# Optimization experiments

Measured on AMD Instinct MI355X. Metric: run time of the kernel, lower is better.

## Reference

```python
import jax, jax.numpy as jnp
import numpy as np

B, L1, L2, H, A = 32, 512, 512, 256, 256

def setup_inputs() -> dict:
    key = jax.random.key(0)
    ks = jax.random.split(key, 10)
    s = 0.05
    return {
        'x1': jax.random.normal(ks[0], (B, L1, H), jnp.float32),
        'x2': jax.random.normal(ks[1], (B, L2, H), jnp.float32),
        'w1': jax.random.normal(ks[2], (A, H), jnp.float32) * s,
        'w2': jax.random.normal(ks[3], (A, H), jnp.float32) * s,
        'D': jax.random.normal(ks[4], (A, A), jnp.float32) * s,
        'W': jax.random.normal(ks[5], (L1, L2), jnp.float32) * s,
        'gru_wih': jax.random.normal(ks[6], (3 * H, 2 * H), jnp.float32) * s,
        'gru_whh': jax.random.normal(ks[7], (3 * H, H), jnp.float32) * s,
        'gru_bih': jax.random.normal(ks[8], (3 * H,), jnp.float32) * s,
        'gru_bhh': jax.random.normal(ks[9], (3 * H,), jnp.float32) * s,
    }

def _gru(seq, wih, whh, bih, bhh):
    # seq: [B, T, 2H]; PyTorch GRU gate order: r, z, n
    h_dim = whh.shape[1]
    x_proj = seq @ wih.T + bih  # [B, T, 3H]
    x_proj = jnp.swapaxes(x_proj, 0, 1)  # [T, B, 3H]
    h0 = jnp.zeros((seq.shape[0], h_dim), seq.dtype)

    def step(h, xp):
        hp = h @ whh.T + bhh  # [B, 3H]
        xr, xz, xn = jnp.split(xp, 3, axis=-1)
        hr, hz, hn = jnp.split(hp, 3, axis=-1)
        r = jax.nn.sigmoid(xr + hr)
        z = jax.nn.sigmoid(xz + hz)
        n = jnp.tanh(xn + r * hn)
        h_new = (1.0 - z) * n + z * h
        return h_new, h_new

    _, out = jax.lax.scan(step, h0, x_proj)
    return jnp.swapaxes(out, 0, 1)  # [B, T, H]

def reference(x1, x2, w1, w2, D, W, gru_wih, gru_whh, gru_bih, gru_bhh):
    a1 = jax.nn.relu(x1 @ w1.T)            # [B, L1, A]
    a2 = jax.nn.relu(x2 @ w2.T)            # [B, L2, A]
    a1 = a1 @ D                             # [B, L1, A]
    M = jnp.einsum('bia,bja->bij', a1, a2)  # [B, L1, L2]
    M = M * W[None, :, :]
    M = jax.nn.softmax(M, axis=1)           # softmax over len1 axis (dim=1)
    ctx = jnp.einsum('bij,bjh->bih', M, x2) # [B, L1, H]
    g = jnp.concatenate([x1, ctx], axis=2)  # [B, L1, 2H]
    return _gru(g, gru_wih, gru_whh, gru_bih, gru_bhh)
```

## Files before the change

kernel.cpp:

```cpp
#include <hip/hip_runtime.h>
#include <hip/hip_bf16.h>
#include <cstdint>
#include <cstddef>


typedef short s8v __attribute__((ext_vector_type(8)));
typedef float f4v __attribute__((ext_vector_type(4)));
typedef _Float16 h8v __attribute__((ext_vector_type(8)));

#if __has_builtin(__builtin_amdgcn_sched_barrier)
#define SCHED_FENCE() __builtin_amdgcn_sched_barrier(0)
#else
#define SCHED_FENCE() asm volatile("" ::: "memory")
#endif

__device__ __forceinline__ void bar_lds() {
    asm volatile("s_waitcnt lgkmcnt(0)\n\ts_barrier" ::: "memory");
}

__device__ __forceinline__ float fast_exp(float x) {
#if __has_builtin(__builtin_amdgcn_exp2f)
    return __builtin_amdgcn_exp2f(x * 1.44269504f);
#else
    return __expf(x);
#endif
}
__device__ __forceinline__ float fast_rcp(float x) {
#if __has_builtin(__builtin_amdgcn_rcpf)
    return __builtin_amdgcn_rcpf(x);
#else
    return 1.f / x;
#endif
}
__device__ __forceinline__ float fast_sig(float x) { return fast_rcp(1.f + fast_exp(-x)); }
__device__ __forceinline__ float fast_tanh(float x) {
    return 1.f - 2.f * fast_rcp(1.f + fast_exp(2.f * x));
}

__global__ __launch_bounds__(256) void gemm_bf16(
    const __hip_bfloat16* __restrict__ A, int lda, long long sA,
    const __hip_bfloat16* __restrict__ B, int ldb, long long sB,
    void* __restrict__ C, int ldc, long long sC,
    int K,
    const float* __restrict__ bias,
    const float* __restrict__ emul, int ldmul,
    int relu, int accum, int out_bf16)
{
    __shared__ short As[128][40];
    __shared__ short Bs[128][40];

    const int tid  = threadIdx.x;
    const int wave = tid >> 6, lane = tid & 63;
    const int quad = lane >> 4, l16 = lane & 15;
    const int wrow = (wave >> 1) * 64, wcol = (wave & 1) * 64;
    const int m0 = blockIdx.y * 128, n0 = blockIdx.x * 128;

    const short* Ab = (const short*)A + (size_t)blockIdx.z * sA;
    const short* Bb = (const short*)B + (size_t)blockIdx.z * sB;

    f4v acc[4][4];
#pragma unroll
    for (int i = 0; i < 4; ++i)
#pragma unroll
        for (int j = 0; j < 4; ++j) acc[i][j] = 0.f;

    const int r0 = tid >> 2,        s0 = (tid & 3) * 8;
    const int r1 = (tid + 256) >> 2, s1 = ((tid + 256) & 3) * 8;

    for (int k0 = 0; k0 < K; k0 += 32) {
        *(s8v*)&As[r0][s0] = *(const s8v*)(Ab + (size_t)(m0 + r0) * lda + k0 + s0);
        *(s8v*)&As[r1][s1] = *(const s8v*)(Ab + (size_t)(m0 + r1) * lda + k0 + s1);
        *(s8v*)&Bs[r0][s0] = *(const s8v*)(Bb + (size_t)(n0 + r0) * ldb + k0 + s0);
        *(s8v*)&Bs[r1][s1] = *(const s8v*)(Bb + (size_t)(n0 + r1) * ldb + k0 + s1);
        __syncthreads();

        s8v af[4], bf[4];
#pragma unroll
        for (int i = 0; i < 4; ++i)
            af[i] = *(const s8v*)&As[wrow + i * 16 + l16][quad * 8];
#pragma unroll
        for (int j = 0; j < 4; ++j)
            bf[j] = *(const s8v*)&Bs[wcol + j * 16 + l16][quad * 8];
#pragma unroll
        for (int i = 0; i < 4; ++i)
#pragma unroll
            for (int j = 0; j < 4; ++j)
                acc[i][j] = __builtin_amdgcn_mfma_f32_16x16x32_bf16(
                    af[i], bf[j], acc[i][j], 0, 0, 0);
        __syncthreads();
    }

    float* Cf = (float*)C + (size_t)blockIdx.z * sC;
    __hip_bfloat16* Cb = (__hip_bfloat16*)C + (size_t)blockIdx.z * sC;
#pragma unroll
    for (int i = 0; i < 4; ++i)
#pragma unroll
        for (int j = 0; j < 4; ++j)
#pragma unroll
            for (int r = 0; r < 4; ++r) {
                const int m = m0 + wrow + i * 16 + quad * 4 + r;
                const int n = n0 + wcol + j * 16 + l16;
                float v = acc[i][j][r];
                if (bias)  v += bias[n];
                if (accum) v += Cf[(size_t)m * ldc + n];
                if (emul)  v *= emul[(size_t)m * ldmul + n];
                if (relu)  v = fmaxf(v, 0.f);
                if (out_bf16) Cb[(size_t)m * ldc + n] = __float2bfloat16(v);
                else          Cf[(size_t)m * ldc + n] = v;
            }
}

__global__ __launch_bounds__(256) void gemm_M(
    const __hip_bfloat16* __restrict__ A,
    const __hip_bfloat16* __restrict__ B,
    __hip_bfloat16* __restrict__ E,
    const float* __restrict__ Wm,
    float* __restrict__ S)
{
    __shared__ short As[128][40];
    __shared__ short Bs[128][40];

    const int tid  = threadIdx.x;
    const int wave = tid >> 6, lane = tid & 63;
    const int quad = lane >> 4, l16 = lane & 15;
    const int wrow = (wave >> 1) * 64, wcol = (wave & 1) * 64;
    const int m0 = blockIdx.y * 128, n0 = blockIdx.x * 128;

    const short* Ab = (const short*)A + (size_t)blockIdx.z * 131072;
    const short* Bb = (const short*)B + (size_t)blockIdx.z * 131072;

    f4v acc[4][4];
#pragma unroll
    for (int i = 0; i < 4; ++i)
#pragma unroll
        for (int j = 0; j < 4; ++j) acc[i][j] = 0.f;

    const int r0 = tid >> 2,        s0 = (tid & 3) * 8;
    const int r1 = (tid + 256) >> 2, s1 = ((tid + 256) & 3) * 8;

    for (int k0 = 0; k0 < 256; k0 += 32) {
        *(s8v*)&As[r0][s0] = *(const s8v*)(Ab + (size_t)(m0 + r0) * 256 + k0 + s0);
        *(s8v*)&As[r1][s1] = *(const s8v*)(Ab + (size_t)(m0 + r1) * 256 + k0 + s1);
        *(s8v*)&Bs[r0][s0] = *(const s8v*)(Bb + (size_t)(n0 + r0) * 256 + k0 + s0);
        *(s8v*)&Bs[r1][s1] = *(const s8v*)(Bb + (size_t)(n0 + r1) * 256 + k0 + s1);
        __syncthreads();

        s8v af[4], bf[4];
#pragma unroll
        for (int i = 0; i < 4; ++i)
            af[i] = *(const s8v*)&As[wrow + i * 16 + l16][quad * 8];
#pragma unroll
        for (int j = 0; j < 4; ++j)
            bf[j] = *(const s8v*)&Bs[wcol + j * 16 + l16][quad * 8];
#pragma unroll
        for (int i = 0; i < 4; ++i)
#pragma unroll
            for (int j = 0; j < 4; ++j)
                acc[i][j] = __builtin_amdgcn_mfma_f32_16x16x32_bf16(
                    af[i], bf[j], acc[i][j], 0, 0, 0);
        __syncthreads();
    }

    __hip_bfloat16* Eb = E + (size_t)blockIdx.z * 262144;
    float* Sb = S + blockIdx.z * 512;
#pragma unroll
    for (int j = 0; j < 4; ++j) {
        const int n = n0 + wcol + j * 16 + l16;
        float colsum = 0.f;
#pragma unroll
        for (int i = 0; i < 4; ++i)
#pragma unroll
            for (int r = 0; r < 4; ++r) {
                const int m = m0 + wrow + i * 16 + quad * 4 + r;
                float v = acc[i][j][r] * Wm[(size_t)m * 512 + n];
                float e = __expf(v);
                colsum += e;
                Eb[(size_t)m * 512 + n] = __float2bfloat16(e);
            }
        atomicAdd(&Sb[n], colsum);
    }
}

__global__ __launch_bounds__(256) void gemm_xp(
    const __hip_bfloat16* __restrict__ A1,
    const __hip_bfloat16* __restrict__ A2,
    const __hip_bfloat16* __restrict__ B,
    float* __restrict__ C,
    const float* __restrict__ bias)
{
    __shared__ short As[128][40];
    __shared__ short Bs[128][40];

    const int tid  = threadIdx.x;
    const int wave = tid >> 6, lane = tid & 63;
    const int quad = lane >> 4, l16 = lane & 15;
    const int wrow = (wave >> 1) * 64, wcol = (wave & 1) * 64;
    const int m0 = blockIdx.y * 128, n0 = blockIdx.x * 128;

    f4v acc[4][4];
#pragma unroll
    for (int i = 0; i < 4; ++i)
#pragma unroll
        for (int j = 0; j < 4; ++j) acc[i][j] = 0.f;

    const int r0 = tid >> 2,        s0 = (tid & 3) * 8;
    const int r1 = (tid + 256) >> 2, s1 = ((tid + 256) & 3) * 8;

    for (int k0 = 0; k0 < 512; k0 += 32) {
        const short* Ab = (const short*)(k0 < 256 ? A1 : A2);
        const int ka = k0 & 255;
        *(s8v*)&As[r0][s0] = *(const s8v*)(Ab + (size_t)(m0 + r0) * 256 + ka + s0);
        *(s8v*)&As[r1][s1] = *(const s8v*)(Ab + (size_t)(m0 + r1) * 256 + ka + s1);
        *(s8v*)&Bs[r0][s0] = *(const s8v*)((const short*)B + (size_t)(n0 + r0) * 512 + k0 + s0);
        *(s8v*)&Bs[r1][s1] = *(const s8v*)((const short*)B + (size_t)(n0 + r1) * 512 + k0 + s1);
        __syncthreads();

        s8v af[4], bf[4];
#pragma unroll
        for (int i = 0; i < 4; ++i)
            af[i] = *(const s8v*)&As[wrow + i * 16 + l16][quad * 8];
#pragma unroll
        for (int j = 0; j < 4; ++j)
            bf[j] = *(const s8v*)&Bs[wcol + j * 16 + l16][quad * 8];
#pragma unroll
        for (int i = 0; i < 4; ++i)
#pragma unroll
            for (int j = 0; j < 4; ++j)
                acc[i][j] = __builtin_amdgcn_mfma_f32_16x16x32_bf16(
                    af[i], bf[j], acc[i][j], 0, 0, 0);
        __syncthreads();
    }

#pragma unroll
    for (int i = 0; i < 4; ++i)
#pragma unroll
        for (int j = 0; j < 4; ++j)
#pragma unroll
            for (int r = 0; r < 4; ++r) {
                const int m = m0 + wrow + i * 16 + quad * 4 + r;
                const int n = n0 + wcol + j * 16 + l16;
                C[(size_t)m * 768 + n] = acc[i][j][r] + bias[n];
            }
}

__global__ __launch_bounds__(256) void prolog(
    const float* __restrict__ x1, const float* __restrict__ x2,
    const float* __restrict__ w1, const float* __restrict__ w2,
    const float* __restrict__ Dm,
    __hip_bfloat16* __restrict__ x1b, __hip_bfloat16* __restrict__ x2b,
    __hip_bfloat16* __restrict__ x2tb,
    __hip_bfloat16* __restrict__ w1b, __hip_bfloat16* __restrict__ w2b,
    __hip_bfloat16* __restrict__ Dtb,
    float* __restrict__ S)
{
    __shared__ float t[32][33];
    const int blk = blockIdx.x, tid = threadIdx.x;

    if (blk < 4096) {
        const int i = (blk * 256 + tid) * 4;
        float4 v = *(const float4*)(x1 + i);
        x1b[i + 0] = __float2bfloat16(v.x);
        x1b[i + 1] = __float2bfloat16(v.y);
        x1b[i + 2] = __float2bfloat16(v.z);
        x1b[i + 3] = __float2bfloat16(v.w);
    } else if (blk < 8192) {
        const int idx = blk - 4096;
        const int bz = idx >> 7, by = (idx >> 3) & 15, bx = idx & 7;
        const int r0 = by * 32, c0 = bx * 32;
        const int tx = tid & 31, ty = tid >> 5;
        const float* Sx = x2 + (size_t)bz * 131072;
        __hip_bfloat16* Dc = x2b + (size_t)bz * 131072;
        __hip_bfloat16* Dd = x2tb + (size_t)bz * 131072;
#pragma unroll
        for (int i = 0; i < 32; i += 8) {
            const size_t idx2 = (size_t)(r0 + ty + i) * 256 + c0 + tx;
            float v = Sx[idx2];
            t[ty + i][tx] = v;
            Dc[idx2] = __float2bfloat16(v);
        }
        __syncthreads();
#pragma unroll
        for (int i = 0; i < 32; i += 8)
            Dd[(size_t)(c0 + ty + i) * 512 + r0 + tx] = __float2bfloat16(t[tx][ty + i]);
    } else if (blk < 8320) {
        const int gid = (blk - 8192) * 256 + tid;
        if (gid < 4096)
            *(float4*)(S + gid * 4) = make_float4(0.f, 0.f, 0.f, 0.f);
        const int i = gid * 4;
        const float* s;
        __hip_bfloat16* d;
        if (i < 65536) { s = w1 + i;           d = w1b + i; }
        else           { s = w2 + (i - 65536); d = w2b + (i - 65536); }
        float4 v = *(const float4*)s;
        d[0] = __float2bfloat16(v.x);
        d[1] = __float2bfloat16(v.y);
        d[2] = __float2bfloat16(v.z);
        d[3] = __float2bfloat16(v.w);
    } else {
        const int idx = blk - 8320;
        const int by = idx >> 3, bx = idx & 7;
        const int r0 = by * 32, c0 = bx * 32;
        const int tx = tid & 31, ty = tid >> 5;
#pragma unroll
        for (int i = 0; i < 32; i += 8)
            t[ty + i][tx] = Dm[(size_t)(r0 + ty + i) * 256 + c0 + tx];
        __syncthreads();
#pragma unroll
        for (int i = 0; i < 32; i += 8)
            Dtb[(size_t)(c0 + ty + i) * 256 + r0 + tx] = __float2bfloat16(t[tx][ty + i]);
    }
}

__global__ __launch_bounds__(256) void post_M(
    const float* __restrict__ wih, __hip_bfloat16* __restrict__ wihb,
    __hip_bfloat16* __restrict__ X, const float* __restrict__ S)
{
    const int blk = blockIdx.x, tid = threadIdx.x;
    if (blk < 384) {
        const int i = (blk * 256 + tid) * 4;
        float4 v = *(const float4*)(wih + i);
        wihb[i + 0] = __float2bfloat16(v.x);
        wihb[i + 1] = __float2bfloat16(v.y);
        wihb[i + 2] = __float2bfloat16(v.z);
        wihb[i + 3] = __float2bfloat16(v.w);
    } else {
        const size_t tt = (size_t)(blk - 384) * 256 + tid;
        const size_t e0 = tt * 8;
        const int j0 = (int)(e0 & 511);
        const int b  = (int)(e0 >> 17);
        const float* Sb = S + b * 512 + j0;
        union { s8v v; __hip_bfloat16 h[8]; } u;
        u.v = *(const s8v*)(X + e0);
#pragma unroll
        for (int k = 0; k < 8; ++k)
            u.h[k] = __float2bfloat16(__bfloat162float(u.h[k]) / Sb[k]);
        *(s8v*)(X + e0) = u.v;
    }
}

__global__ __launch_bounds__(512, 2)
void gru_kernel(
    const float* __restrict__ xproj,
    const float* __restrict__ whh,
    const float* __restrict__ bhh,
    float* __restrict__ out)
{
    const int b    = blockIdx.x;
    const int tid  = threadIdx.x;
    const int wave = tid >> 6, lane = tid & 63;
    const int quad = lane >> 4, l16 = lane & 15;

    __shared__ __align__(16) _Float16 hhf[256];
    __shared__ __align__(16) float    hp[768];

    h8v wreg[6][8];
#pragma unroll
    for (int i = 0; i < 6; ++i) {
        const float* rp = whh + (size_t)(96 * wave + 16 * i + l16) * 256 + quad * 8;
#pragma unroll
        for (int kk = 0; kk < 8; ++kk) {
            float4 t0 = *(const float4*)(rp + kk * 32);
            float4 t1 = *(const float4*)(rp + kk * 32 + 4);
            h8v f;
            f[0] = (_Float16)t0.x; f[1] = (_Float16)t0.y;
            f[2] = (_Float16)t0.z; f[3] = (_Float16)t0.w;
            f[4] = (_Float16)t1.x; f[5] = (_Float16)t1.y;
            f[6] = (_Float16)t1.z; f[7] = (_Float16)t1.w;
            wreg[i][kk] = f;
        }
    }

    const float* xb = xproj + (size_t)b * 512 * 768;
    float*       ob = out   + (size_t)b * 512 * 256;

    float hA = 0.f, xr = 0.f, xz = 0.f, xn = 0.f;
    float br = 0.f, bz = 0.f, bn = 0.f;
    if (tid < 256) {
        br = bhh[tid]; bz = bhh[256 + tid]; bn = bhh[512 + tid];
        xr = xb[tid];  xz = xb[256 + tid];  xn = xb[512 + tid];
        hhf[tid] = (_Float16)0.f;
    }
    bar_lds();

    for (int t = 0; t < 512; ++t) {
        float nxr = 0.f, nxz = 0.f, nxn = 0.f;
        if (tid < 256) {
            const float* xpn = xb + (size_t)((t + 1) & 511) * 768;
            nxr = xpn[tid]; nxz = xpn[256 + tid]; nxn = xpn[512 + tid];
        }

        f4v acc[6];
#pragma unroll
        for (int i = 0; i < 6; ++i) acc[i] = 0.f;

        h8v bf_cur = *(const h8v*)&hhf[quad * 8];
#pragma unroll
        for (int kk = 0; kk < 8; ++kk) {
            h8v bf_nxt = bf_cur;
            if (kk < 7) bf_nxt = *(const h8v*)&hhf[(kk + 1) * 32 + quad * 8];
#pragma unroll
            for (int i = 0; i < 6; ++i)
                acc[i] = __builtin_amdgcn_mfma_f32_16x16x32_f16(
                    wreg[i][kk], bf_cur, acc[i], 0, 0, 0);
            SCHED_FENCE();
            bf_cur = bf_nxt;
        }

        if (l16 == 0) {
#pragma unroll
            for (int i = 0; i < 6; ++i)
                *(f4v*)&hp[96 * wave + 16 * i + 4 * quad] = acc[i];
        }
        bar_lds();

        if (tid < 256) {
            float hr = hp[tid]       + br;
            float hz = hp[256 + tid] + bz;
            float hn = hp[512 + tid] + bn;
            float r = fast_sig(xr + hr);
            float z = fast_sig(xz + hz);
            float n = fast_tanh(xn + r * hn);
            float h = (1.f - z) * n + z * hA;
            hA = h;
            hhf[tid] = (_Float16)h;
            ob[(size_t)t * 256 + tid] = h;
            xr = nxr; xz = nxz; xn = nxn;
        }
        bar_lds();
    }
}

extern "C" void kernel_launch(void* const* d_in, const int* in_sizes, int n_in,
                              void* d_out, int out_size, void* d_ws, size_t ws_size,
                              hipStream_t stream)
{
    (void)in_sizes; (void)n_in; (void)out_size; (void)ws_size;

    const float* x1  = (const float*)d_in[0];
    const float* x2  = (const float*)d_in[1];
    const float* w1  = (const float*)d_in[2];
    const float* w2  = (const float*)d_in[3];
    const float* Dm  = (const float*)d_in[4];
    const float* Wm  = (const float*)d_in[5];
    const float* wih = (const float*)d_in[6];
    const float* whh = (const float*)d_in[7];
    const float* bih = (const float*)d_in[8];
    const float* bhh = (const float*)d_in[9];
    float* out = (float*)d_out;

    char* base = (char*)d_ws;
    __hip_bfloat16* w1b  = (__hip_bfloat16*)(base + 0);
    __hip_bfloat16* w2b  = (__hip_bfloat16*)(base + 131072);
    __hip_bfloat16* Dtb  = (__hip_bfloat16*)(base + 262144);
    float*          Ssum = (float*)(base + 1048576);
    float*          xp   = (float*)(base + 0);
    __hip_bfloat16* a1db = (__hip_bfloat16*)(base + 8388608);
    __hip_bfloat16* a1b  = (__hip_bfloat16*)(base + 33554432);
    __hip_bfloat16* Msb  = (__hip_bfloat16*)(base + 33554432);
    __hip_bfloat16* x1b  = (__hip_bfloat16*)(base + 50331648);
    __hip_bfloat16* x2b  = (__hip_bfloat16*)(base + 58720256);
    __hip_bfloat16* ctxb = (__hip_bfloat16*)(base + 58720256);
    __hip_bfloat16* x2tb = (__hip_bfloat16*)(base + 67108864);
    __hip_bfloat16* a2b  = (__hip_bfloat16*)(base + 75497472);
    __hip_bfloat16* wihb = (__hip_bfloat16*)(base + 75497472);

    dim3 blk(256);

    prolog<<<dim3(8384), blk, 0, stream>>>(
        x1, x2, w1, w2, Dm, x1b, x2b, x2tb, w1b, w2b, Dtb, Ssum);

    gemm_bf16<<<dim3(2, 128, 2), blk, 0, stream>>>(
        x1b, 256, 4194304, w1b, 256, 65536, a1b, 256, 20971520, 256,
        nullptr, nullptr, 0, 1, 0, 1);
    gemm_bf16<<<dim3(2, 128, 1), blk, 0, stream>>>(
        a1b, 256, 0, Dtb, 256, 0, a1db, 256, 0, 256,
        nullptr, nullptr, 0, 0, 0, 1);
    gemm_M<<<dim3(4, 4, 32), blk, 0, stream>>>(a1db, a2b, Msb, Wm, Ssum);
    post_M<<<dim3(2432), blk, 0, stream>>>(wih, wihb, x2tb, Ssum);
    gemm_bf16<<<dim3(2, 4, 32), blk, 0, stream>>>(
        Msb, 512, 262144, x2tb, 512, 131072, ctxb, 256, 131072, 512,
        nullptr, nullptr, 0, 0, 0, 1);
    gemm_xp<<<dim3(6, 128, 1), blk, 0, stream>>>(x1b, ctxb, wihb, xp, bih);
    gru_kernel<<<dim3(32), dim3(512), 0, stream>>>(xp, whh, bhh, out);
}
```

Baseline: 855.0 us.

## Remap GRU gate rows per wave to drop LDS round-trip and barrier

Each wave now owns matching r/z/n rows for the same 32 hidden units, so the gate update can read the MFMA accumulators straight from registers. This removes the hp shared buffer and one of the two barriers per timestep. The hidden state in LDS is double-buffered so the single remaining barrier is enough. Fewer lanes (8 of 16 per quad group) do the elementwise gate math, and selecting from the accumulators adds some VALU work.

```diff
diff --git a/kernel.cpp b/kernel.cpp
--- a/kernel.cpp
+++ b/kernel.cpp
@@ -35,6 +35,12 @@
 __device__ __forceinline__ float fast_sig(float x) { return fast_rcp(1.f + fast_exp(-x)); }
 __device__ __forceinline__ float fast_tanh(float x) {
     return 1.f - 2.f * fast_rcp(1.f + fast_exp(2.f * x));
+}
+
+__device__ __forceinline__ float sel4(f4v v, int rr) {
+    float a = (rr & 1) ? v[1] : v[0];
+    float b = (rr & 1) ? v[3] : v[2];
+    return (rr & 2) ? b : a;
 }
 
 __global__ __launch_bounds__(256) void gemm_bf16(
@@ -350,13 +356,17 @@
     const int wave = tid >> 6, lane = tid & 63;
     const int quad = lane >> 4, l16 = lane & 15;
 
-    __shared__ __align__(16) _Float16 hhf[256];
-    __shared__ __align__(16) float    hp[768];
+    __shared__ __align__(16) _Float16 hhf[2][256];
+
+    const int w32 = 32 * wave;
+    const int rowb[6] = { w32, w32 + 16,
+                          256 + w32, 256 + w32 + 16,
+                          512 + w32, 512 + w32 + 16 };
 
     h8v wreg[6][8];
 #pragma unroll
     for (int i = 0; i < 6; ++i) {
-        const float* rp = whh + (size_t)(96 * wave + 16 * i + l16) * 256 + quad * 8;
+        const float* rp = whh + (size_t)(rowb[i] + l16) * 256 + quad * 8;
 #pragma unroll
         for (int kk = 0; kk < 8; ++kk) {
             float4 t0 = *(const float4*)(rp + kk * 32);
@@ -373,31 +383,37 @@
     const float* xb = xproj + (size_t)b * 512 * 768;
     float*       ob = out   + (size_t)b * 512 * 256;
 
+    const bool act = (l16 < 8);
+    const int g  = (l16 >> 2) & 1;
+    const int rr = l16 & 3;
+    const int e  = w32 + 16 * g + 4 * quad + rr;
+
     float hA = 0.f, xr = 0.f, xz = 0.f, xn = 0.f;
     float br = 0.f, bz = 0.f, bn = 0.f;
-    if (tid < 256) {
-        br = bhh[tid]; bz = bhh[256 + tid]; bn = bhh[512 + tid];
-        xr = xb[tid];  xz = xb[256 + tid];  xn = xb[512 + tid];
-        hhf[tid] = (_Float16)0.f;
-    }
+    if (act) {
+        br = bhh[e]; bz = bhh[256 + e]; bn = bhh[512 + e];
+        xr = xb[e];  xz = xb[256 + e];  xn = xb[512 + e];
+    }
+    if (tid < 256) hhf[0][tid] = (_Float16)0.f;
     bar_lds();
 
     for (int t = 0; t < 512; ++t) {
         float nxr = 0.f, nxz = 0.f, nxn = 0.f;
-        if (tid < 256) {
+        if (act) {
             const float* xpn = xb + (size_t)((t + 1) & 511) * 768;
-            nxr = xpn[tid]; nxz = xpn[256 + tid]; nxn = xpn[512 + tid];
+            nxr = xpn[e]; nxz = xpn[256 + e]; nxn = xpn[512 + e];
         }
 
         f4v acc[6];
 #pragma unroll
         for (int i = 0; i < 6; ++i) acc[i] = 0.f;
 
-        h8v bf_cur = *(const h8v*)&hhf[quad * 8];
+        const _Float16* hc = hhf[t & 1];
+        h8v bf_cur = *(const h8v*)&hc[quad * 8];
 #pragma unroll
         for (int kk = 0; kk < 8; ++kk) {
             h8v bf_nxt = bf_cur;
-            if (kk < 7) bf_nxt = *(const h8v*)&hhf[(kk + 1) * 32 + quad * 8];
+            if (kk < 7) bf_nxt = *(const h8v*)&hc[(kk + 1) * 32 + quad * 8];
 #pragma unroll
             for (int i = 0; i < 6; ++i)
                 acc[i] = __builtin_amdgcn_mfma_f32_16x16x32_f16(
@@ -406,25 +422,23 @@
             bf_cur = bf_nxt;
         }
 
-        if (l16 == 0) {
-#pragma unroll
-            for (int i = 0; i < 6; ++i)
-                *(f4v*)&hp[96 * wave + 16 * i + 4 * quad] = acc[i];
-        }
-        bar_lds();
-
-        if (tid < 256) {
-            float hr = hp[tid]       + br;
-            float hz = hp[256 + tid] + bz;
-            float hn = hp[512 + tid] + bn;
-            float r = fast_sig(xr + hr);
-            float z = fast_sig(xz + hz);
-            float n = fast_tanh(xn + r * hn);
-            float h = (1.f - z) * n + z * hA;
-            hA = h;
-            hhf[tid] = (_Float16)h;
-            ob[(size_t)t * 256 + tid] = h;
-            xr = nxr; xz = nxz; xn = nxn;
+        {
+            f4v vr = g ? acc[1] : acc[0];
+            f4v vz = g ? acc[3] : acc[2];
+            f4v vn = g ? acc[5] : acc[4];
+            float hpr = sel4(vr, rr);
+            float hpz = sel4(vz, rr);
+            float hpn = sel4(vn, rr);
+            if (act) {
+                float r = fast_sig(xr + br + hpr);
+                float z = fast_sig(xz + bz + hpz);
+                float n = fast_tanh(xn + r * (hpn + bn));
+                float h = (1.f - z) * n + z * hA;
+                hA = h;
+                hhf[(t + 1) & 1][e] = (_Float16)h;
+                ob[(size_t)t * 256 + e] = h;
+                xr = nxr; xz = nxz; xn = nxn;
+            }
         }
         bar_lds();
     }
```

After: 712.9 us (median of 2 runs). -16.6%, faster.
